# Performance work log

Hardware: AMD Instinct MI355X
Metric: run time of the kernel (lower is better)

Reference implementation:

```python
import jax, jax.numpy as jnp
import numpy as np

B, S, T, H, E, VIN, VOUT = 2048, 24, 25, 256, 300, 64, 128


def gru_cell(x, h, Wih, Whh, bih, bhh):
    # PyTorch GRU gate order: r, z, n
    gi = x @ Wih + bih          # [B, 3H]
    gh = h @ Whh + bhh          # [B, 3H]
    hd = h.shape[-1]
    ir, iz, in_ = gi[:, :hd], gi[:, hd:2 * hd], gi[:, 2 * hd:]
    hr, hz, hn = gh[:, :hd], gh[:, hd:2 * hd], gh[:, 2 * hd:]
    r = jax.nn.sigmoid(ir + hr)
    z = jax.nn.sigmoid(iz + hz)
    n = jnp.tanh(in_ + r * hn)
    return (1.0 - z) * n + z * h


def setup_inputs() -> dict:
    key = jax.random.key(0)
    ks = jax.random.split(key, 26)
    it = iter(range(26))

    def p(shape):
        return jax.random.normal(ks[next(it)], shape, jnp.float32) * 0.05

    src = jax.random.randint(ks[next(it)], (S, B), 0, VIN)
    trg = jax.random.randint(ks[next(it)], (T, B), 0, VOUT)
    return dict(
        src=src, trg=trg,
        enc_emb=p((VIN, E)),
        enc_Wih_f=p((E, 3 * H)), enc_Whh_f=p((H, 3 * H)), enc_bih_f=p((3 * H,)), enc_bhh_f=p((3 * H,)),
        enc_Wih_b=p((E, 3 * H)), enc_Whh_b=p((H, 3 * H)), enc_bih_b=p((3 * H,)), enc_bhh_b=p((3 * H,)),
        enc_fcW=p((2 * H, H)), enc_fcb=p((H,)),
        attn_Wh=p((H, H)), attn_We=p((2 * H, H)), attn_b=p((H,)), attn_v=p((H,)),
        dec_emb=p((VOUT, E)),
        dec_Wih=p((E + 2 * H, 3 * H)), dec_Whh=p((H, 3 * H)), dec_bih=p((3 * H,)), dec_bhh=p((3 * H,)),
        fcW=p((H + 2 * H + E, VOUT)), fcb=p((VOUT,)),
        teacher_forcing_ratio=1,
    )


def reference(src, trg, enc_emb, enc_Wih_f, enc_Whh_f, enc_bih_f, enc_bhh_f,
              enc_Wih_b, enc_Whh_b, enc_bih_b, enc_bhh_b, enc_fcW, enc_fcb,
              attn_Wh, attn_We, attn_b, attn_v, dec_emb,
              dec_Wih, dec_Whh, dec_bih, dec_bhh, fcW, fcb,
              teacher_forcing_ratio):
    # ---- Encoder: bidirectional single-layer GRU ----
    x = enc_emb[src]                                   # [S, B, E]
    h0 = jnp.zeros((x.shape[1], H), x.dtype)

    def mk(Wih, Whh, bih, bhh):
        def step(h, xt):
            hn = gru_cell(xt, h, Wih, Whh, bih, bhh)
            return hn, hn
        return step

    hf, out_f = jax.lax.scan(mk(enc_Wih_f, enc_Whh_f, enc_bih_f, enc_bhh_f), h0, x)
    hb, out_b = jax.lax.scan(mk(enc_Wih_b, enc_Whh_b, enc_bih_b, enc_bhh_b), h0, x[::-1])
    enc_out = jnp.concatenate([out_f, out_b[::-1]], axis=-1)   # [S, B, 2H]
    hidden = jnp.tanh(jnp.concatenate([hf, hb], axis=-1) @ enc_fcW + enc_fcb)  # [B, H]

    # ---- Decoder: teacher-forced loop (teacher_forcing_ratio=1 => deterministic) ----
    enc_bse = enc_out.transpose(1, 0, 2)               # [B, S, 2H]
    enc_proj = enc_bse @ attn_We                       # [B, S, H] (hoisted linear part of attn)
    embed_seq = dec_emb[trg[:-1]]                      # [T-1, B, E]

    def dec_step(h, emb_t):
        energy = jnp.tanh((h @ attn_Wh)[:, None, :] + enc_proj + attn_b)  # [B, S, H]
        a = jax.nn.softmax(energy @ attn_v, axis=-1)                      # [B, S]
        weighted = jnp.einsum('bs,bsd->bd', a, enc_bse)                   # [B, 2H]
        xg = jnp.concatenate([emb_t, weighted], axis=-1)                  # [B, E+2H]
        hn = gru_cell(xg, h, dec_Wih, dec_Whh, dec_bih, dec_bhh)          # [B, H]
        logits = jnp.concatenate([hn, weighted, emb_t], axis=-1) @ fcW + fcb
        return hn, logits

    _, logits = jax.lax.scan(dec_step, hidden, embed_seq)  # [T-1, B, VOUT]
    outputs = jnp.concatenate(
        [jnp.zeros((1,) + logits.shape[1:], logits.dtype), logits], axis=0)  # [T, B, VOUT]
    return outputs
```

## Files before the change

### kernel.cpp

```cpp
#include <hip/hip_runtime.h>
#include <hip/hip_bf16.h>

typedef __hip_bfloat16 bf16;
typedef __attribute__((ext_vector_type(8))) short short8;
typedef __attribute__((ext_vector_type(4))) float f32x4;

__device__ __forceinline__ float to_f(float x) { return x; }
__device__ __forceinline__ float to_f(bf16 x) { return __bfloat162float(x); }
__device__ __forceinline__ float ldp(const void* p, size_t i, bool f32) {
  return f32 ? ((const float*)p)[i] : __bfloat162float(((const bf16*)p)[i]);
}
__device__ __forceinline__ short f2b(float f) {
  bf16 h = __float2bfloat16(f);
  return *reinterpret_cast<short*>(&h);
}
__device__ __forceinline__ int perm1024(int c) {
  return ((c & 255) >> 4) * 64 + (c >> 8) * 16 + (c & 15);
}

__global__ void detect_kernel(const void* __restrict__ probe,
                              unsigned* __restrict__ flag) {
  __shared__ int sbad;
  if (threadIdx.x == 0) sbad = 0;
  __syncthreads();
  const unsigned short* u = (const unsigned short*)probe;
  int bad = 0;
  for (int i = threadIdx.x; i < 2048; i += 256) {
    unsigned short w = u[i];
    unsigned e = (w >> 7) & 0xFFu;
    bool plaus = (w == 0) || (w == 0x8000u) || (e >= 0x60u && e <= 0x7Eu);
    if (!plaus) bad++;
  }
  atomicAdd(&sbad, bad);
  __syncthreads();
  if (threadIdx.x == 0) *flag = (sbad > 100) ? 1u : 0u;
}

#define MAXSEG 24
struct PrepArgs {
  int nseg;
  const void* src[MAXSEG];
  long long soff[MAXSEG];
  short* dst[MAXSEG];
  int scols[MAXSEG];
  int dstride[MAXSEG];
  int transp[MAXSEG];
  long long prefix[MAXSEG + 1];
};
__global__ void prep_kernel(PrepArgs a, const unsigned* __restrict__ dflag) {
  const bool isf32 = (*dflag != 0u);
  long long i = (long long)blockIdx.x * 256 + threadIdx.x;
  if (i >= a.prefix[a.nseg]) return;
  int s = 0;
  while (i >= a.prefix[s + 1]) s++;
  long long loc = i - a.prefix[s];
  long long r = loc / a.scols[s], c = loc % a.scols[s];
  float v = a.src[s] ? ldp(a.src[s], (size_t)(a.soff[s] + loc), isf32) : 0.f;
  int tp = a.transp[s];
  long long idx;
  if (tp == 1)
    idx = c * a.dstride[s] + r;
  else if (tp == 2)
    idx = (long long)perm1024((int)c) * a.dstride[s] + r;
  else if (tp == 3)
    idx = perm1024((int)c);
  else
    idx = r * a.dstride[s] + c;
  a.dst[s][idx] = f2b(v);
}

struct GJob {
  const bf16* A;
  const short* WT;
  const bf16* bias;
  float* Cf;
  bf16* Ch;
  const float* Cin;
  const int* cinrow;
  int lda, wst, K, M, N, flags;
};
struct GJobs {
  GJob j[4];
};

__global__ __launch_bounds__(256) void mj_gemm(GJobs args) {
  GJob jb = args.j[blockIdx.z];
  const int n0 = blockIdx.x * 128, m0 = blockIdx.y * 128;
  if (n0 >= jb.N || m0 >= jb.M) return;
  __shared__ short As[128][40];
  __shared__ short Bs[128][40];
  const int tid = threadIdx.x, lane = tid & 63, wave = tid >> 6;
  const int srow = tid >> 1, skoff = (tid & 1) * 16;
  const int wr = (wave >> 1) * 64, wc = (wave & 1) * 64;

  const short* abase =
      (const short*)jb.A + (long long)(m0 + srow) * jb.lda + skoff;
  const short* bbase = jb.WT + (long long)(n0 + srow) * jb.wst + skoff;

  f32x4 acc[4][4];
#pragma unroll
  for (int i = 0; i < 4; i++)
#pragma unroll
    for (int j = 0; j < 4; j++) acc[i][j] = 0.f;

  const int K = jb.K;
  short8 a0 = *(const short8*)(abase);
  short8 a1 = *(const short8*)(abase + 8);
  short8 b0 = *(const short8*)(bbase);
  short8 b1 = *(const short8*)(bbase + 8);

  for (int k0 = 0; k0 < K; k0 += 32) {
    __syncthreads();
    *(short8*)&As[srow][skoff] = a0;
    *(short8*)&As[srow][skoff + 8] = a1;
    *(short8*)&Bs[srow][skoff] = b0;
    *(short8*)&Bs[srow][skoff + 8] = b1;
    __syncthreads();
    int kn = (k0 + 32 < K) ? k0 + 32 : k0;
    a0 = *(const short8*)(abase + kn);
    a1 = *(const short8*)(abase + kn + 8);
    b0 = *(const short8*)(bbase + kn);
    b1 = *(const short8*)(bbase + kn + 8);
    short8 af[4], bfr[4];
#pragma unroll
    for (int i = 0; i < 4; i++)
      af[i] = *(short8*)&As[wr + i * 16 + (lane & 15)][(lane >> 4) * 8];
#pragma unroll
    for (int j = 0; j < 4; j++)
      bfr[j] = *(short8*)&Bs[wc + j * 16 + (lane & 15)][(lane >> 4) * 8];
#pragma unroll
    for (int i = 0; i < 4; i++)
#pragma unroll
      for (int j = 0; j < 4; j++)
        acc[i][j] =
            __builtin_amdgcn_mfma_f32_16x16x32_bf16(af[i], bfr[j], acc[i][j],
                                                    0, 0, 0);
  }

  const int N = jb.N;
  const float* cin = jb.Cin;
  const int* cri = jb.cinrow;
#pragma unroll
  for (int j = 0; j < 4; j++) {
    int col = n0 + wc + j * 16 + (lane & 15);
    float bv = jb.bias ? to_f(jb.bias[col]) : 0.f;
#pragma unroll
    for (int i = 0; i < 4; i++) {
#pragma unroll
      for (int r = 0; r < 4; r++) {
        int row = m0 + wr + i * 16 + (lane >> 4) * 4 + r;
        float v = acc[i][j][r] + bv;
        if (cin) {
          long long crow = cri ? (long long)cri[row] : (long long)row;
          v += cin[crow * N + col];
        }
        if (jb.flags & 4) v = tanhf(v);
        if (jb.Cf) jb.Cf[(long long)row * N + col] = v;
        if (jb.Ch) jb.Ch[(long long)row * N + col] = __float2bfloat16(v);
      }
    }
  }
}

struct CJob {
  const bf16* A;
  const short* WT;
  const bf16* bias;
  const bf16* gh;
  const int* tok;
  const bf16* giTab;
  float* hF;
  bf16* hBf;
  bf16* out2;
  long long out2s;
  int lda, wst, K, hstride, hoff;
};
struct CJobs {
  CJob j[2];
};

__global__ __launch_bounds__(256) void mj_gemm_cell(CJobs args) {
  CJob jb = args.j[blockIdx.z];
  const int n0 = blockIdx.x * 128, m0 = blockIdx.y * 128;
  __shared__ short As[128][40];
  __shared__ short Bs[128][40];
  __shared__ int toks[128];
  const int tid = threadIdx.x, lane = tid & 63, wave = tid >> 6;
  const int srow = tid >> 1, skoff = (tid & 1) * 16;
  const int wr = (wave >> 1) * 64, wcq = (wave & 1) * 64;

  if (tid < 128) toks[tid] = jb.tok[m0 + tid];
  const short* abase =
      (const short*)jb.A + (long long)(m0 + srow) * jb.lda + skoff;
  const short* bbase = jb.WT + (long long)(n0 + srow) * jb.wst + skoff;

  f32x4 acc[4][4];
#pragma unroll
  for (int i = 0; i < 4; i++)
#pragma unroll
    for (int j = 0; j < 4; j++) acc[i][j] = 0.f;

  const int K = jb.K;
  short8 a0 = *(const short8*)(abase);
  short8 a1 = *(const short8*)(abase + 8);
  short8 b0 = *(const short8*)(bbase);
  short8 b1 = *(const short8*)(bbase + 8);

  for (int k0 = 0; k0 < K; k0 += 32) {
    __syncthreads();
    *(short8*)&As[srow][skoff] = a0;
    *(short8*)&As[srow][skoff + 8] = a1;
    *(short8*)&Bs[srow][skoff] = b0;
    *(short8*)&Bs[srow][skoff + 8] = b1;
    __syncthreads();
    int kn = (k0 + 32 < K) ? k0 + 32 : k0;
    a0 = *(const short8*)(abase + kn);
    a1 = *(const short8*)(abase + kn + 8);
    b0 = *(const short8*)(bbase + kn);
    b1 = *(const short8*)(bbase + kn + 8);
    short8 af[4], bfr[4];
#pragma unroll
    for (int i = 0; i < 4; i++)
      af[i] = *(short8*)&As[wr + i * 16 + (lane & 15)][(lane >> 4) * 8];
#pragma unroll
    for (int j = 0; j < 4; j++)
      bfr[j] = *(short8*)&Bs[wcq + j * 16 + (lane & 15)][(lane >> 4) * 8];
#pragma unroll
    for (int i = 0; i < 4; i++)
#pragma unroll
      for (int j = 0; j < 4; j++)
        acc[i][j] =
            __builtin_amdgcn_mfma_f32_16x16x32_bf16(af[i], bfr[j], acc[i][j],
                                                    0, 0, 0);
  }

  const int u = lane & 15, hi4 = (lane >> 4) * 4;
  const int i_h = ((n0 + wcq) >> 6) * 16 + u;
  float b0g = 0.f, b1g = 0.f, b2g = 0.f;
  if (jb.bias) {
    b0g = to_f(jb.bias[n0 + wcq + u]);
    b1g = to_f(jb.bias[n0 + wcq + 16 + u]);
    b2g = to_f(jb.bias[n0 + wcq + 32 + u]);
  }
#pragma unroll
  for (int i = 0; i < 4; i++) {
#pragma unroll
    for (int r = 0; r < 4; r++) {
      int row = m0 + wr + i * 16 + hi4 + r;
      const bf16* gi = jb.giTab + (long long)toks[row - m0] * 768 + i_h;
      float t0 = to_f(gi[0]), t1 = to_f(gi[256]), t2 = to_f(gi[512]);
      float g0 = acc[i][0][r] + b0g, g1 = acc[i][1][r] + b1g,
            g2 = acc[i][2][r] + b2g;
      float ir, iz, in_, hr, hz, hn;
      if (jb.gh) {
        const bf16* gb = jb.gh + (long long)row * 1024 + i_h;
        ir = g0 + t0;
        iz = g1 + t1;
        in_ = g2 + t2;
        hr = to_f(gb[0]);
        hz = to_f(gb[256]);
        hn = to_f(gb[512]);
      } else {
        ir = t0;
        iz = t1;
        in_ = t2;
        hr = g0;
        hz = g1;
        hn = g2;
      }
      long long hidx = (long long)row * jb.hstride + jb.hoff + i_h;
      float hv = jb.hF[hidx];
      float rr = 1.f / (1.f + expf(-(ir + hr)));
      float zz = 1.f / (1.f + expf(-(iz + hz)));
      float nn = tanhf(in_ + rr * hn);
      float o = (1.f - zz) * nn + zz * hv;
      jb.hF[hidx] = o;
      jb.hBf[hidx] = __float2bfloat16(o);
      jb.out2[(long long)row * jb.out2s + i_h] = __float2bfloat16(o);
    }
  }
}

__global__ __launch_bounds__(256) void attn_kernel(
    const bf16* __restrict__ ghw, const bf16* __restrict__ proj,
    const bf16* __restrict__ bse, const void* __restrict__ v,
    bf16* __restrict__ xgc, const unsigned* __restrict__ dflag) {
  const bool isf32 = (*dflag != 0u);
  int b = blockIdx.x, tid = threadIdx.x;
  int wave = tid >> 6, lane = tid & 63;
  __shared__ float partial[24][4];
  __shared__ float aw[24];
  float vh = to_f(ghw[(long long)b * 1024 + 768 + tid]);
  float vv = ldp(v, tid, isf32);
  const bf16* pb = proj + (long long)b * 24 * 256;
#pragma unroll 4
  for (int s = 0; s < 24; s++) {
    float e = tanhf(vh + __bfloat162float(pb[s * 256 + tid]));
    float t = vv * e;
#pragma unroll
    for (int off = 32; off > 0; off >>= 1) t += __shfl_down(t, off, 64);
    if (lane == 0) partial[s][wave] = t;
  }
  __syncthreads();
  if (tid == 0) {
    float sc[24];
    float mx = -1e30f;
    for (int s = 0; s < 24; s++) {
      float xv = partial[s][0] + partial[s][1] + partial[s][2] + partial[s][3];
      sc[s] = xv;
      mx = fmaxf(mx, xv);
    }
    float sum = 0.f;
    for (int s = 0; s < 24; s++) {
      sc[s] = expf(sc[s] - mx);
      sum += sc[s];
    }
    float inv = 1.f / sum;
    for (int s = 0; s < 24; s++) aw[s] = sc[s] * inv;
  }
  __syncthreads();
  const bf16* eb = bse + (long long)b * 24 * 512;
  float w0 = 0.f, w1 = 0.f;
#pragma unroll 4
  for (int s = 0; s < 24; s++) {
    float a = aw[s];
    w0 += a * __bfloat162float(eb[s * 512 + tid]);
    w1 += a * __bfloat162float(eb[s * 512 + 256 + tid]);
  }
  bf16* xb = xgc + (long long)b * 768;
  xb[tid] = __float2bfloat16(w0);
  xb[256 + tid] = __float2bfloat16(w1);
}

__global__ void sentinel_kernel(float* out, int n) {
  int i = blockIdx.x * 256 + threadIdx.x;
  if (i < n) out[i] = 123.0f;
}

extern "C" void kernel_launch(void* const* d_in, const int* in_sizes, int n_in,
                              void* d_out, int out_size, void* d_ws,
                              size_t ws_size, hipStream_t stream) {
  const int B = 2048, S = 24, T = 25, VOUT = 128;
  const int* src = (const int*)d_in[0];
  const int* trg = (const int*)d_in[1];
  const void* enc_emb = d_in[2];
  const void* enc_Wih_f = d_in[3];
  const void* enc_Whh_f = d_in[4];
  const void* enc_bih_f = d_in[5];
  const void* enc_bhh_f = d_in[6];
  const void* enc_Wih_b = d_in[7];
  const void* enc_Whh_b = d_in[8];
  const void* enc_bih_b = d_in[9];
  const void* enc_bhh_b = d_in[10];
  const void* enc_fcW = d_in[11];
  const void* enc_fcb = d_in[12];
  const void* attn_Wh = d_in[13];
  const void* attn_We = d_in[14];
  const void* attn_b = d_in[15];
  const void* attn_v = d_in[16];
  const void* dec_emb = d_in[17];
  const void* dec_Wih = d_in[18];
  const void* dec_Whh = d_in[19];
  const void* dec_bih = d_in[20];
  const void* dec_bhh = d_in[21];
  const void* fcW = d_in[22];
  const void* fcb = d_in[23];
  float* out = (float*)d_out;

  size_t need = 0;
  auto place = [&](size_t bytes) {
    size_t off = need;
    need += (bytes + 255) & ~(size_t)255;
    return off;
  };
  size_t o_flag = place(256);
  size_t o_wstart = need;
  size_t oEmbE = place(64 * 320 * 2);
  size_t oEmbD = place(128 * 320 * 2);
  size_t oWT1 = place(768 * 320 * 2);
  size_t oWT2 = place(1024 * 256 * 2);
  size_t oWT3 = place(768 * 320 * 2);
  size_t oWT4 = place(1024 * 256 * 2);
  size_t oWT5 = place(256 * 512 * 2);
  size_t oWT6 = place(256 * 512 * 2);
  size_t oWcT = place(1024 * 256 * 2);
  size_t oW7aT = place(768 * 320 * 2);
  size_t oW7bT = place(1024 * 512 * 2);
  size_t oW8aT = place(128 * 320 * 2);
  size_t oW8bT = place(128 * 768 * 2);
  size_t oB1 = place(768 * 2), oB2 = place(1024 * 2);
  size_t oB3 = place(768 * 2), oB4 = place(1024 * 2);
  size_t oB5 = place(256 * 2), oB6 = place(256 * 2);
  size_t oB7 = place(768 * 2), oBc = place(1024 * 2), oB8 = place(128 * 2);
  size_t o_wend = need;
  size_t o_bse = place((size_t)B * S * 512 * 2);
  size_t o_proj = place((size_t)B * S * 256 * 2);
  size_t o_ghw = place((size_t)B * 1024 * 2);
  size_t o_hfb = place((size_t)B * 512 * 4);
  size_t o_hb0 = place((size_t)B * 512 * 2);
  size_t o_hb1 = place((size_t)B * 512 * 2);
  size_t o_hd = place((size_t)B * 256 * 4);
  size_t o_hdbf = place((size_t)B * 256 * 2);
  size_t o_xgc = place((size_t)(T - 1) * B * 768 * 2);
  size_t o_gtF = place(128 * 768 * 2);
  size_t o_gtB = place(128 * 768 * 2);
  size_t o_gtE = place(128 * 768 * 2);
  size_t o_fcT = place(128 * 128 * 4);

  if (ws_size < need) {
    sentinel_kernel<<<(out_size + 255) / 256, 256, 0, stream>>>(out, out_size);
    return;
  }

  char* base = (char*)d_ws;
  unsigned* dflag = (unsigned*)(base + o_flag);
  bf16* embE = (bf16*)(base + oEmbE);
  bf16* embD = (bf16*)(base + oEmbD);
  short* WT1 = (short*)(base + oWT1);
  short* WT2p = (short*)(base + oWT2);
  short* WT3 = (short*)(base + oWT3);
  short* WT4p = (short*)(base + oWT4);
  short* WT5 = (short*)(base + oWT5);
  short* WT6 = (short*)(base + oWT6);
  short* WcT = (short*)(base + oWcT);
  short* W7aT = (short*)(base + oW7aT);
  short* W7bTp = (short*)(base + oW7bT);
  short* W8aT = (short*)(base + oW8aT);
  short* W8bT = (short*)(base + oW8bT);
  bf16 *B1 = (bf16*)(base + oB1), *B2p = (bf16*)(base + oB2);
  bf16 *B3 = (bf16*)(base + oB3), *B4p = (bf16*)(base + oB4);
  bf16 *B5 = (bf16*)(base + oB5), *B6 = (bf16*)(base + oB6);
  bf16 *B7 = (bf16*)(base + oB7), *Bc = (bf16*)(base + oBc);
  bf16* B8 = (bf16*)(base + oB8);
  bf16* bse = (bf16*)(base + o_bse);
  bf16* proj = (bf16*)(base + o_proj);
  bf16* ghw = (bf16*)(base + o_ghw);
  float* hfb = (float*)(base + o_hfb);
  bf16* hb[2] = {(bf16*)(base + o_hb0), (bf16*)(base + o_hb1)};
  float* h_d = (float*)(base + o_hd);
  bf16* hdbf = (bf16*)(base + o_hdbf);
  bf16* xgcAll = (bf16*)(base + o_xgc);
  bf16* giTabF = (bf16*)(base + o_gtF);
  bf16* giTabB = (bf16*)(base + o_gtB);
  bf16* giTabE = (bf16*)(base + o_gtE);
  float* fcTab = (float*)(base + o_fcT);

  detect_kernel<<<1, 256, 0, stream>>>(enc_emb, dflag);
  (void)hipMemsetAsync(base + o_wstart, 0, o_wend - o_wstart, stream);

  PrepArgs pa;
  int ns = 0;
  long long tot = 0;
  auto seg = [&](const void* s, long long soff, short* dst, int scols,
                 int dstride, int transp, long long count) {
    pa.src[ns] = s;
    pa.soff[ns] = soff;
    pa.dst[ns] = dst;
    pa.scols[ns] = scols;
    pa.dstride[ns] = dstride;
    pa.transp[ns] = transp;
    pa.prefix[ns] = tot;
    tot += count;
    ns++;
  };
  seg(enc_emb, 0, (short*)embE, 300, 320, 0, 64 * 300);
  seg(dec_emb, 0, (short*)embD, 300, 320, 0, 128 * 300);
  seg(enc_Wih_f, 0, WT1, 768, 320, 1, 230400);
  seg(enc_Whh_f, 0, WT2p, 768, 256, 2, 196608);
  seg(enc_Wih_b, 0, WT3, 768, 320, 1, 230400);
  seg(enc_Whh_b, 0, WT4p, 768, 256, 2, 196608);
  seg(enc_fcW, 0, WT5, 256, 512, 1, 131072);
  seg(attn_We, 0, WT6, 256, 512, 1, 131072);
  seg(dec_Whh, 0, WcT, 768, 256, 1, 196608);
  seg(attn_Wh, 0, WcT + 768 * 256, 256, 256, 1, 65536);
  seg(dec_Wih, 0, W7aT, 768, 320, 1, 300 * 768);
  seg(dec_Wih, (long long)300 * 768, W7bTp, 768, 512, 2, 512 * 768);
  seg(fcW, (long long)768 * 128, W8aT, 128, 320, 1, 300 * 128);
  seg(fcW, (long long)256 * 128, W8bT, 128, 768, 1, 512 * 128);
  seg(fcW, 0, W8bT + 512, 128, 768, 1, 256 * 128);
  seg(enc_bih_f, 0, (short*)B1, 768, 768, 0, 768);
  seg(enc_bhh_f, 0, (short*)B2p, 768, 1024, 3, 768);
  seg(enc_bih_b, 0, (short*)B3, 768, 768, 0, 768);
  seg(enc_bhh_b, 0, (short*)B4p, 768, 1024, 3, 768);
  seg(enc_fcb, 0, (short*)B5, 256, 256, 0, 256);
  seg(attn_b, 0, (short*)B6, 256, 256, 0, 256);
  seg(dec_bih, 0, (short*)B7, 768, 768, 0, 768);
  seg(dec_bhh, 0, (short*)Bc, 768, 768, 0, 768);
  seg(fcb, 0, (short*)B8, 128, 128, 0, 128);
  pa.prefix[ns] = tot;
  pa.nseg = ns;
  prep_kernel<<<(int)((tot + 255) / 256), 256, 0, stream>>>(pa, dflag);

  (void)hipMemsetAsync(hfb, 0, (size_t)B * 512 * 4, stream);
  (void)hipMemsetAsync(hb[0], 0, (size_t)B * 512 * 2, stream);
  (void)hipMemsetAsync(out, 0, (size_t)B * VOUT * 4, stream);

  auto launch = [&](const GJob* jobs, int nj, int gx, int gy) {
    GJobs a{};
    for (int i = 0; i < nj; i++) a.j[i] = jobs[i];
    mj_gemm<<<dim3(gx, gy, nj), 256, 0, stream>>>(a);
  };
  auto launchC = [&](const CJob* jobs, int nj) {
    CJobs a{};
    for (int i = 0; i < nj; i++) a.j[i] = jobs[i];
    mj_gemm_cell<<<dim3(8, 16, nj), 256, 0, stream>>>(a);
  };

  {
    GJob tj[4];
    tj[0] = {embE, WT1, B1, nullptr, giTabF, nullptr, nullptr,
             320, 320, 320, 128, 768, 0};
    tj[1] = {embE, WT3, B3, nullptr, giTabB, nullptr, nullptr,
             320, 320, 320, 128, 768, 0};
    tj[2] = {embD, W7aT, B7, nullptr, giTabE, nullptr, nullptr,
             320, 320, 320, 128, 768, 0};
    tj[3] = {embD, W8aT, B8, fcTab, nullptr, nullptr, nullptr,
             320, 320, 320, 128, 128, 0};
    launch(tj, 4, 6, 1);
  }

  for (int s = 0; s < S; s++) {
    CJob c[2];
    c[0] = {hb[s & 1], WT2p, B2p, nullptr, src + (size_t)s * B, giTabF,
            hfb, hb[(s + 1) & 1], bse + (size_t)s * 512, 12288,
            512, 256, 256, 512, 0};
    c[1] = {hb[s & 1] + 256, WT4p, B4p, nullptr,
            src + (size_t)(S - 1 - s) * B, giTabB,
            hfb, hb[(s + 1) & 1], bse + (size_t)(S - 1 - s) * 512 + 256, 12288,
            512, 256, 256, 512, 256};
    launchC(c, 2);
  }

  {
    GJob mj[2];
    mj[0] = {hb[0], WT5, B5, h_d, hdbf, nullptr, nullptr,
             512, 512, 512, B, 256, 4};
    mj[1] = {bse, WT6, B6, nullptr, proj, nullptr, nullptr,
             512, 512, 512, B * S, 256, 0};
    launch(mj, 2, 2, 384);
  }

  auto wc_job = [&]() -> GJob {
    return {hdbf, WcT, Bc, nullptr, ghw, nullptr, nullptr,
            256, 256, 256, B, 1024, 0};
  };
  {
    GJob j0 = wc_job();
    launch(&j0, 1, 8, 16);
  }
  for (int t = 0; t < T - 1; t++) {
    bf16* xr = xgcAll + (size_t)t * B * 768;
    attn_kernel<<<B, 256, 0, stream>>>(ghw, proj, bse, attn_v, xr, dflag);
    CJob c = {xr, W7bTp, nullptr, ghw, trg + (size_t)t * B, giTabE,
              h_d, hdbf, xr + 512, 768, 768, 512, 512, 256, 0};
    launchC(&c, 1);
    if (t < T - 2) {
      GJob j0 = wc_job();
      launch(&j0, 1, 8, 16);
    }
  }
  {
    GJob jf = {xgcAll, W8bT, nullptr, out + (size_t)B * VOUT, nullptr,
               fcTab, trg, 768, 768, 768, (T - 1) * B, 128, 0};
    launch(&jf, 1, 1, 384);
  }
}
```

Before: 2.190 ms.

## Precompute attention-weighted input projections and fuse decoder cell with next Whh GEMM

Uses linearity of the attention-weighted context: the context-dependent parts of the GRU input gates and output logits are precomputed over all encoder positions (P7 = bse·W7b, P8 = bse·W8w), so each step only needs an attention-weighted sum instead of a per-step GEMM over the context. The decoder GRU cell now runs inside a new kernel that also computes the next step's Whh/attn_Wh projection and the per-step logits, which removes the separate Wc GEMM launch and the final large FC GEMM. The cost is a much larger one-time precompute and storage of B×S×768 and B×S×128 tensors, plus a fused kernel where each of its 9 column blocks recomputes the cell elementwise work.

```diff
diff --git a/kernel.cpp b/kernel.cpp
--- a/kernel.cpp
+++ b/kernel.cpp
@@ -4,6 +4,9 @@
 typedef __hip_bfloat16 bf16;
 typedef __attribute__((ext_vector_type(8))) short short8;
 typedef __attribute__((ext_vector_type(4))) float f32x4;
+
+#define MFMA(va, vb, vc) \
+  __builtin_amdgcn_mfma_f32_16x16x32_bf16(va, vb, vc, 0, 0, 0)
 
 __device__ __forceinline__ float to_f(float x) { return x; }
 __device__ __forceinline__ float to_f(bf16 x) { return __bfloat162float(x); }
@@ -75,8 +78,6 @@
   const bf16* bias;
   float* Cf;
   bf16* Ch;
-  const float* Cin;
-  const int* cinrow;
   int lda, wst, K, M, N, flags;
 };
 struct GJobs {
@@ -96,27 +97,24 @@
   const short* abase =
       (const short*)jb.A + (long long)(m0 + srow) * jb.lda + skoff;
   const short* bbase = jb.WT + (long long)(n0 + srow) * jb.wst + skoff;
-
   f32x4 acc[4][4];
 #pragma unroll
   for (int i = 0; i < 4; i++)
 #pragma unroll
     for (int j = 0; j < 4; j++) acc[i][j] = 0.f;
 
-  const int K = jb.K;
   short8 a0 = *(const short8*)(abase);
   short8 a1 = *(const short8*)(abase + 8);
   short8 b0 = *(const short8*)(bbase);
   short8 b1 = *(const short8*)(bbase + 8);
-
-  for (int k0 = 0; k0 < K; k0 += 32) {
+  for (int k0 = 0; k0 < jb.K; k0 += 32) {
     __syncthreads();
     *(short8*)&As[srow][skoff] = a0;
     *(short8*)&As[srow][skoff + 8] = a1;
     *(short8*)&Bs[srow][skoff] = b0;
     *(short8*)&Bs[srow][skoff + 8] = b1;
     __syncthreads();
-    int kn = (k0 + 32 < K) ? k0 + 32 : k0;
+    int kn = (k0 + 32 < jb.K) ? k0 + 32 : k0;
     a0 = *(const short8*)(abase + kn);
     a1 = *(const short8*)(abase + kn + 8);
     b0 = *(const short8*)(bbase + kn);
@@ -131,15 +129,9 @@
 #pragma unroll
     for (int i = 0; i < 4; i++)
 #pragma unroll
-      for (int j = 0; j < 4; j++)
-        acc[i][j] =
-            __builtin_amdgcn_mfma_f32_16x16x32_bf16(af[i], bfr[j], acc[i][j],
-                                                    0, 0, 0);
-  }
-
+      for (int j = 0; j < 4; j++) acc[i][j] = MFMA(af[i], bfr[j], acc[i][j]);
+  }
   const int N = jb.N;
-  const float* cin = jb.Cin;
-  const int* cri = jb.cinrow;
 #pragma unroll
   for (int j = 0; j < 4; j++) {
     int col = n0 + wc + j * 16 + (lane & 15);
@@ -150,10 +142,6 @@
       for (int r = 0; r < 4; r++) {
         int row = m0 + wr + i * 16 + (lane >> 4) * 4 + r;
         float v = acc[i][j][r] + bv;
-        if (cin) {
-          long long crow = cri ? (long long)cri[row] : (long long)row;
-          v += cin[crow * N + col];
-        }
         if (jb.flags & 4) v = tanhf(v);
         if (jb.Cf) jb.Cf[(long long)row * N + col] = v;
         if (jb.Ch) jb.Ch[(long long)row * N + col] = __float2bfloat16(v);
@@ -166,7 +154,6 @@
   const bf16* A;
   const short* WT;
   const bf16* bias;
-  const bf16* gh;
   const int* tok;
   const bf16* giTab;
   float* hF;
@@ -200,20 +187,18 @@
 #pragma unroll
     for (int j = 0; j < 4; j++) acc[i][j] = 0.f;
 
-  const int K = jb.K;
   short8 a0 = *(const short8*)(abase);
   short8 a1 = *(const short8*)(abase + 8);
   short8 b0 = *(const short8*)(bbase);
   short8 b1 = *(const short8*)(bbase + 8);
-
-  for (int k0 = 0; k0 < K; k0 += 32) {
+  for (int k0 = 0; k0 < jb.K; k0 += 32) {
     __syncthreads();
     *(short8*)&As[srow][skoff] = a0;
     *(short8*)&As[srow][skoff + 8] = a1;
     *(short8*)&Bs[srow][skoff] = b0;
     *(short8*)&Bs[srow][skoff + 8] = b1;
     __syncthreads();
-    int kn = (k0 + 32 < K) ? k0 + 32 : k0;
+    int kn = (k0 + 32 < jb.K) ? k0 + 32 : k0;
     a0 = *(const short8*)(abase + kn);
     a1 = *(const short8*)(abase + kn + 8);
     b0 = *(const short8*)(bbase + kn);
@@ -228,46 +213,24 @@
 #pragma unroll
     for (int i = 0; i < 4; i++)
 #pragma unroll
-      for (int j = 0; j < 4; j++)
-        acc[i][j] =
-            __builtin_amdgcn_mfma_f32_16x16x32_bf16(af[i], bfr[j], acc[i][j],
-                                                    0, 0, 0);
+      for (int j = 0; j < 4; j++) acc[i][j] = MFMA(af[i], bfr[j], acc[i][j]);
   }
 
   const int u = lane & 15, hi4 = (lane >> 4) * 4;
   const int i_h = ((n0 + wcq) >> 6) * 16 + u;
-  float b0g = 0.f, b1g = 0.f, b2g = 0.f;
-  if (jb.bias) {
-    b0g = to_f(jb.bias[n0 + wcq + u]);
-    b1g = to_f(jb.bias[n0 + wcq + 16 + u]);
-    b2g = to_f(jb.bias[n0 + wcq + 32 + u]);
-  }
+  const float b0g = to_f(jb.bias[n0 + wcq + u]);
+  const float b1g = to_f(jb.bias[n0 + wcq + 16 + u]);
+  const float b2g = to_f(jb.bias[n0 + wcq + 32 + u]);
 #pragma unroll
   for (int i = 0; i < 4; i++) {
 #pragma unroll
     for (int r = 0; r < 4; r++) {
       int row = m0 + wr + i * 16 + hi4 + r;
       const bf16* gi = jb.giTab + (long long)toks[row - m0] * 768 + i_h;
-      float t0 = to_f(gi[0]), t1 = to_f(gi[256]), t2 = to_f(gi[512]);
-      float g0 = acc[i][0][r] + b0g, g1 = acc[i][1][r] + b1g,
-            g2 = acc[i][2][r] + b2g;
-      float ir, iz, in_, hr, hz, hn;
-      if (jb.gh) {
-        const bf16* gb = jb.gh + (long long)row * 1024 + i_h;
-        ir = g0 + t0;
-        iz = g1 + t1;
-        in_ = g2 + t2;
-        hr = to_f(gb[0]);
-        hz = to_f(gb[256]);
-        hn = to_f(gb[512]);
-      } else {
-        ir = t0;
-        iz = t1;
-        in_ = t2;
-        hr = g0;
-        hz = g1;
-        hn = g2;
-      }
+      float ir = to_f(gi[0]), iz = to_f(gi[256]), in_ = to_f(gi[512]);
+      float hr = acc[i][0][r] + b0g;
+      float hz = acc[i][1][r] + b1g;
+      float hn = acc[i][2][r] + b2g;
       long long hidx = (long long)row * jb.hstride + jb.hoff + i_h;
       float hv = jb.hF[hidx];
       float rr = 1.f / (1.f + expf(-(ir + hr)));
@@ -281,21 +244,28 @@
   }
 }
 
-__global__ __launch_bounds__(256) void attn_kernel(
-    const bf16* __restrict__ ghw, const bf16* __restrict__ proj,
-    const bf16* __restrict__ bse, const void* __restrict__ v,
-    bf16* __restrict__ xgc, const unsigned* __restrict__ dflag) {
-  const bool isf32 = (*dflag != 0u);
+struct AttnPArgs {
+  const bf16* ghw;
+  const bf16* proj;
+  const bf16* P7;
+  const bf16* P8w;
+  const void* v;
+  const unsigned* dflag;
+  bf16* gi_dyn;
+  float* l8;
+};
+__global__ __launch_bounds__(256) void attnp_kernel(AttnPArgs a) {
   int b = blockIdx.x, tid = threadIdx.x;
   int wave = tid >> 6, lane = tid & 63;
   __shared__ float partial[24][4];
   __shared__ float aw[24];
-  float vh = to_f(ghw[(long long)b * 1024 + 768 + tid]);
-  float vv = ldp(v, tid, isf32);
-  const bf16* pb = proj + (long long)b * 24 * 256;
+  const bool isf32 = (*a.dflag != 0u);
+  float vh = to_f(a.ghw[(long long)b * 1024 + 768 + tid]);
+  float vv = ldp(a.v, tid, isf32);
+  const bf16* pb = a.proj + (long long)b * 24 * 256;
 #pragma unroll 4
   for (int s = 0; s < 24; s++) {
-    float e = tanhf(vh + __bfloat162float(pb[s * 256 + tid]));
+    float e = tanhf(vh + to_f(pb[s * 256 + tid]));
     float t = vv * e;
 #pragma unroll
     for (int off = 32; off > 0; off >>= 1) t += __shfl_down(t, off, 64);
@@ -319,17 +289,105 @@
     for (int s = 0; s < 24; s++) aw[s] = sc[s] * inv;
   }
   __syncthreads();
-  const bf16* eb = bse + (long long)b * 24 * 512;
-  float w0 = 0.f, w1 = 0.f;
+  const bf16* p7 = a.P7 + (long long)b * 24 * 768;
+  float g0 = 0.f, g1 = 0.f, g2 = 0.f;
 #pragma unroll 4
   for (int s = 0; s < 24; s++) {
-    float a = aw[s];
-    w0 += a * __bfloat162float(eb[s * 512 + tid]);
-    w1 += a * __bfloat162float(eb[s * 512 + 256 + tid]);
-  }
-  bf16* xb = xgc + (long long)b * 768;
-  xb[tid] = __float2bfloat16(w0);
-  xb[256 + tid] = __float2bfloat16(w1);
+    float aa = aw[s];
+    g0 += aa * to_f(p7[s * 768 + tid]);
+    g1 += aa * to_f(p7[s * 768 + 256 + tid]);
+    g2 += aa * to_f(p7[s * 768 + 512 + tid]);
+  }
+  bf16* gd = a.gi_dyn + (long long)b * 768;
+  gd[tid] = __float2bfloat16(g0);
+  gd[256 + tid] = __float2bfloat16(g1);
+  gd[512 + tid] = __float2bfloat16(g2);
+  if (tid < 128) {
+    const bf16* p8 = a.P8w + (long long)b * 24 * 128;
+    float l = 0.f;
+#pragma unroll 4
+    for (int s = 0; s < 24; s++) l += aw[s] * to_f(p8[s * 128 + tid]);
+    a.l8[(long long)b * 128 + tid] = l;
+  }
+}
+
+struct CWArgs {
+  const bf16* gi_dyn;
+  const bf16* giTabE;
+  const bf16* ghw_in;
+  bf16* ghw_out;
+  const float* hd_in;
+  float* hd_out;
+  const short* WcT;
+  const bf16* Bc;
+  const short* W8hn;
+  const float* l8;
+  const float* fcTab;
+  const int* trg_t;
+  float* outT;
+};
+__global__ __launch_bounds__(256) void cellwc_kernel(CWArgs a) {
+  const int n0 = blockIdx.x * 128;
+  const int m0 = blockIdx.y * 128;
+  const int tid = threadIdx.x, lane = tid & 63, wave = tid >> 6;
+  const int u = lane & 15, kq = lane >> 4;
+  __shared__ short hA[128][264];
+  __shared__ int toks[128];
+  if (tid < 128) toks[tid] = a.trg_t[m0 + tid];
+  __syncthreads();
+  const int d = tid;
+#pragma unroll 2
+  for (int r = 0; r < 128; r++) {
+    const int row = m0 + r;
+    const bf16* gd = a.gi_dyn + (long long)row * 768;
+    const bf16* ge = a.giTabE + (long long)toks[r] * 768;
+    const bf16* gh = a.ghw_in + (long long)row * 1024;
+    float ir = to_f(gd[d]) + to_f(ge[d]);
+    float iz = to_f(gd[256 + d]) + to_f(ge[256 + d]);
+    float in_ = to_f(gd[512 + d]) + to_f(ge[512 + d]);
+    float hr = to_f(gh[d]), hz = to_f(gh[256 + d]), hn = to_f(gh[512 + d]);
+    float hv = a.hd_in[(long long)row * 256 + d];
+    float rr = 1.f / (1.f + expf(-(ir + hr)));
+    float zz = 1.f / (1.f + expf(-(iz + hz)));
+    float nn = tanhf(in_ + rr * hn);
+    float o = (1.f - zz) * nn + zz * hv;
+    hA[r][d] = f2b(o);
+    if (n0 == 0) a.hd_out[(long long)row * 256 + d] = o;
+  }
+  __syncthreads();
+#pragma unroll
+  for (int nt = 0; nt < 2; nt++) {
+    const int n = n0 + wave * 32 + nt * 16 + u;
+    const short* bp = (n < 1024)
+                          ? a.WcT + (size_t)n * 256 + kq * 8
+                          : a.W8hn + (size_t)(n - 1024) * 256 + kq * 8;
+    short8 bfr[8];
+#pragma unroll
+    for (int kt = 0; kt < 8; kt++) bfr[kt] = *(const short8*)(bp + kt * 32);
+    const bool iswc = (n0 + wave * 32 + nt * 16) < 1024;
+    const float bv = iswc ? to_f(a.Bc[n]) : 0.f;
+#pragma unroll
+    for (int mt = 0; mt < 8; mt++) {
+      f32x4 acc = {0.f, 0.f, 0.f, 0.f};
+#pragma unroll
+      for (int kt = 0; kt < 8; kt++)
+        acc = MFMA(*(const short8*)&hA[mt * 16 + u][kt * 32 + kq * 8],
+                   bfr[kt], acc);
+#pragma unroll
+      for (int r = 0; r < 4; r++) {
+        const int rl = mt * 16 + kq * 4 + r;
+        const int row = m0 + rl;
+        if (iswc) {
+          a.ghw_out[(long long)row * 1024 + n] = __float2bfloat16(acc[r] + bv);
+        } else {
+          const int c = n - 1024;
+          a.outT[(long long)row * 128 + c] =
+              acc[r] + a.l8[(long long)row * 128 + c] +
+              a.fcTab[toks[rl] * 128 + c];
+        }
+      }
+    }
+  }
 }
 
 __global__ void sentinel_kernel(float* out, int n) {
@@ -385,9 +443,10 @@
   size_t oWT6 = place(256 * 512 * 2);
   size_t oWcT = place(1024 * 256 * 2);
   size_t oW7aT = place(768 * 320 * 2);
-  size_t oW7bT = place(1024 * 512 * 2);
+  size_t oW7bT = place(768 * 512 * 2);
   size_t oW8aT = place(128 * 320 * 2);
-  size_t oW8bT = place(128 * 768 * 2);
+  size_t oW8wT = place(128 * 512 * 2);
+  size_t oW8hn = place(128 * 256 * 2);
   size_t oB1 = place(768 * 2), oB2 = place(1024 * 2);
   size_t oB3 = place(768 * 2), oB4 = place(1024 * 2);
   size_t oB5 = place(256 * 2), oB6 = place(256 * 2);
@@ -395,13 +454,18 @@
   size_t o_wend = need;
   size_t o_bse = place((size_t)B * S * 512 * 2);
   size_t o_proj = place((size_t)B * S * 256 * 2);
-  size_t o_ghw = place((size_t)B * 1024 * 2);
+  size_t o_P7 = place((size_t)B * S * 768 * 2);
+  size_t o_P8 = place((size_t)B * S * 128 * 2);
+  size_t o_ghw0 = place((size_t)B * 1024 * 2);
+  size_t o_ghw1 = place((size_t)B * 1024 * 2);
   size_t o_hfb = place((size_t)B * 512 * 4);
   size_t o_hb0 = place((size_t)B * 512 * 2);
   size_t o_hb1 = place((size_t)B * 512 * 2);
-  size_t o_hd = place((size_t)B * 256 * 4);
+  size_t o_hd0 = place((size_t)B * 256 * 4);
+  size_t o_hd1 = place((size_t)B * 256 * 4);
   size_t o_hdbf = place((size_t)B * 256 * 2);
-  size_t o_xgc = place((size_t)(T - 1) * B * 768 * 2);
+  size_t o_gid = place((size_t)B * 768 * 2);
+  size_t o_l8 = place((size_t)B * 128 * 4);
   size_t o_gtF = place(128 * 768 * 2);
   size_t o_gtB = place(128 * 768 * 2);
   size_t o_gtE = place(128 * 768 * 2);
@@ -424,9 +488,10 @@
   short* WT6 = (short*)(base + oWT6);
   short* WcT = (short*)(base + oWcT);
   short* W7aT = (short*)(base + oW7aT);
-  short* W7bTp = (short*)(base + oW7bT);
+  short* W7bT = (short*)(base + oW7bT);
   short* W8aT = (short*)(base + oW8aT);
-  short* W8bT = (short*)(base + oW8bT);
+  short* W8wT = (short*)(base + oW8wT);
+  short* W8hn = (short*)(base + oW8hn);
   bf16 *B1 = (bf16*)(base + oB1), *B2p = (bf16*)(base + oB2);
   bf16 *B3 = (bf16*)(base + oB3), *B4p = (bf16*)(base + oB4);
   bf16 *B5 = (bf16*)(base + oB5), *B6 = (bf16*)(base + oB6);
@@ -434,12 +499,15 @@
   bf16* B8 = (bf16*)(base + oB8);
   bf16* bse = (bf16*)(base + o_bse);
   bf16* proj = (bf16*)(base + o_proj);
-  bf16* ghw = (bf16*)(base + o_ghw);
+  bf16* P7 = (bf16*)(base + o_P7);
+  bf16* P8w = (bf16*)(base + o_P8);
+  bf16* ghw[2] = {(bf16*)(base + o_ghw0), (bf16*)(base + o_ghw1)};
   float* hfb = (float*)(base + o_hfb);
   bf16* hb[2] = {(bf16*)(base + o_hb0), (bf16*)(base + o_hb1)};
-  float* h_d = (float*)(base + o_hd);
+  float* h_d[2] = {(float*)(base + o_hd0), (float*)(base + o_hd1)};
   bf16* hdbf = (bf16*)(base + o_hdbf);
-  bf16* xgcAll = (bf16*)(base + o_xgc);
+  bf16* gi_dyn = (bf16*)(base + o_gid);
+  float* l8 = (float*)(base + o_l8);
   bf16* giTabF = (bf16*)(base + o_gtF);
   bf16* giTabB = (bf16*)(base + o_gtB);
   bf16* giTabE = (bf16*)(base + o_gtE);
@@ -474,10 +542,10 @@
   seg(dec_Whh, 0, WcT, 768, 256, 1, 196608);
   seg(attn_Wh, 0, WcT + 768 * 256, 256, 256, 1, 65536);
   seg(dec_Wih, 0, W7aT, 768, 320, 1, 300 * 768);
-  seg(dec_Wih, (long long)300 * 768, W7bTp, 768, 512, 2, 512 * 768);
+  seg(dec_Wih, (long long)300 * 768, W7bT, 768, 512, 1, 512 * 768);
   seg(fcW, (long long)768 * 128, W8aT, 128, 320, 1, 300 * 128);
-  seg(fcW, (long long)256 * 128, W8bT, 128, 768, 1, 512 * 128);
-  seg(fcW, 0, W8bT + 512, 128, 768, 1, 256 * 128);
+  seg(fcW, (long long)256 * 128, W8wT, 128, 512, 1, 512 * 128);
+  seg(fcW, 0, W8hn, 128, 256, 1, 256 * 128);
   seg(enc_bih_f, 0, (short*)B1, 768, 768, 0, 768);
   seg(enc_bhh_f, 0, (short*)B2p, 768, 1024, 3, 768);
   seg(enc_bih_b, 0, (short*)B3, 768, 768, 0, 768);
@@ -500,68 +568,48 @@
     for (int i = 0; i < nj; i++) a.j[i] = jobs[i];
     mj_gemm<<<dim3(gx, gy, nj), 256, 0, stream>>>(a);
   };
-  auto launchC = [&](const CJob* jobs, int nj) {
-    CJobs a{};
-    for (int i = 0; i < nj; i++) a.j[i] = jobs[i];
-    mj_gemm_cell<<<dim3(8, 16, nj), 256, 0, stream>>>(a);
-  };
 
   {
     GJob tj[4];
-    tj[0] = {embE, WT1, B1, nullptr, giTabF, nullptr, nullptr,
-             320, 320, 320, 128, 768, 0};
-    tj[1] = {embE, WT3, B3, nullptr, giTabB, nullptr, nullptr,
-             320, 320, 320, 128, 768, 0};
-    tj[2] = {embD, W7aT, B7, nullptr, giTabE, nullptr, nullptr,
-             320, 320, 320, 128, 768, 0};
-    tj[3] = {embD, W8aT, B8, fcTab, nullptr, nullptr, nullptr,
-             320, 320, 320, 128, 128, 0};
+    tj[0] = {embE, WT1, B1, nullptr, giTabF, 320, 320, 320, 128, 768, 0};
+    tj[1] = {embE, WT3, B3, nullptr, giTabB, 320, 320, 320, 128, 768, 0};
+    tj[2] = {embD, W7aT, B7, nullptr, giTabE, 320, 320, 320, 128, 768, 0};
+    tj[3] = {embD, W8aT, B8, fcTab, nullptr, 320, 320, 320, 128, 128, 0};
     launch(tj, 4, 6, 1);
   }
 
   for (int s = 0; s < S; s++) {
-    CJob c[2];
-    c[0] = {hb[s & 1], WT2p, B2p, nullptr, src + (size_t)s * B, giTabF,
-            hfb, hb[(s + 1) & 1], bse + (size_t)s * 512, 12288,
-            512, 256, 256, 512, 0};
-    c[1] = {hb[s & 1] + 256, WT4p, B4p, nullptr,
-            src + (size_t)(S - 1 - s) * B, giTabB,
-            hfb, hb[(s + 1) & 1], bse + (size_t)(S - 1 - s) * 512 + 256, 12288,
-            512, 256, 256, 512, 256};
-    launchC(c, 2);
+    CJobs ca{};
+    ca.j[0] = {hb[s & 1], WT2p, B2p, src + (size_t)s * B, giTabF,
+               hfb, hb[(s + 1) & 1], bse + (size_t)s * 512, 12288,
+               512, 256, 256, 512, 0};
+    ca.j[1] = {hb[s & 1] + 256, WT4p, B4p, src + (size_t)(S - 1 - s) * B,
+               giTabB, hfb, hb[(s + 1) & 1],
+               bse + (size_t)(S - 1 - s) * 512 + 256, 12288,
+               512, 256, 256, 512, 256};
+    mj_gemm_cell<<<dim3(8, 16, 2), 256, 0, stream>>>(ca);
   }
 
   {
-    GJob mj[2];
-    mj[0] = {hb[0], WT5, B5, h_d, hdbf, nullptr, nullptr,
-             512, 512, 512, B, 256, 4};
-    mj[1] = {bse, WT6, B6, nullptr, proj, nullptr, nullptr,
-             512, 512, 512, B * S, 256, 0};
-    launch(mj, 2, 2, 384);
-  }
-
-  auto wc_job = [&]() -> GJob {
-    return {hdbf, WcT, Bc, nullptr, ghw, nullptr, nullptr,
-            256, 256, 256, B, 1024, 0};
-  };
+    GJob mj[4];
+    mj[0] = {hb[0], WT5, B5, h_d[0], hdbf, 512, 512, 512, B, 256, 4};
+    mj[1] = {bse, WT6, B6, nullptr, proj, 512, 512, 512, B * S, 256, 0};
+    mj[2] = {bse, W7bT, nullptr, nullptr, P7, 512, 512, 512, B * S, 768, 0};
+    mj[3] = {bse, W8wT, nullptr, nullptr, P8w, 512, 512, 512, B * S, 128, 0};
+    launch(mj, 4, 6, 384);
+  }
   {
-    GJob j0 = wc_job();
+    GJob j0 = {hdbf, WcT, Bc, nullptr, ghw[0], 256, 256, 256, B, 1024, 0};
     launch(&j0, 1, 8, 16);
   }
+
   for (int t = 0; t < T - 1; t++) {
-    bf16* xr = xgcAll + (size_t)t * B * 768;
-    attn_kernel<<<B, 256, 0, stream>>>(ghw, proj, bse, attn_v, xr, dflag);
-    CJob c = {xr, W7bTp, nullptr, ghw, trg + (size_t)t * B, giTabE,
-              h_d, hdbf, xr + 512, 768, 768, 512, 512, 256, 0};
-    launchC(&c, 1);
-    if (t < T - 2) {
-      GJob j0 = wc_job();
-      launch(&j0, 1, 8, 16);
-    }
-  }
-  {
-    GJob jf = {xgcAll, W8bT, nullptr, out + (size_t)B * VOUT, nullptr,
-               fcTab, trg, 768, 768, 768, (T - 1) * B, 128, 0};
-    launch(&jf, 1, 1, 384);
-  }
-}
+    AttnPArgs aa{ghw[t & 1], proj, P7, P8w, attn_v, dflag, gi_dyn, l8};
+    attnp_kernel<<<B, 256, 0, stream>>>(aa);
+    CWArgs cw{gi_dyn,      giTabE, ghw[t & 1],  ghw[(t + 1) & 1],
+              h_d[t & 1],  h_d[(t + 1) & 1],    WcT,  Bc,
+              W8hn,        l8,     fcTab,       trg + (size_t)t * B,
+              out + (size_t)(t + 1) * B * VOUT};
+    cellwc_kernel<<<dim3(9, 16), 256, 0, stream>>>(cw);
+  }
+}
```

Result: slower. 3.519 ms (+60.7%).
